# Performance work log

Measured on AMD Instinct MI355X. Metric: run time of the kernel, lower is better.

## Reference

```python
import jax, jax.numpy as jnp
import numpy as np
from jax import lax

B, CIN, IMG = 32, 3, 128   # batch, image channels, image size
D, K = 256, 512            # codebook dim, codebook size


def _conv(x, w, stride, pad):
    # PyTorch Conv2d (bias=False), NCHW / OIHW
    return lax.conv_general_dilated(x, w, (stride, stride), ((pad, pad), (pad, pad)),
                                    dimension_numbers=('NCHW', 'OIHW', 'NCHW'))


def _deconv(x, w, b):
    # PyTorch ConvTranspose2d(k=4, s=2, p=1): lhs_dilation=2, pad=k-1-p=2, flipped kernel,
    # weight layout (in, out, kh, kw) -> 'IOHW'
    y = lax.conv_general_dilated(x, jnp.flip(w, (2, 3)), (1, 1), ((2, 2), (2, 2)),
                                 lhs_dilation=(2, 2),
                                 dimension_numbers=('NCHW', 'IOHW', 'NCHW'))
    return y + b[None, :, None, None]


def _res(x, w1, w2):
    # Faithful to the source ResidualBlock: relu1 output is DISCARDED (conv1 applied to x)
    out = _conv(x, w1, 1, 1)      # 3x3, pad 1
    out = jax.nn.relu(out)
    out = _conv(out, w2, 1, 0)    # 1x1, pad 0
    return out + x


def setup_inputs() -> dict:
    key = jax.random.key(0)
    ks = jax.random.split(key, 20)
    s = 0.05
    inp = {
        'x': jax.random.uniform(ks[0], (B, CIN, IMG, IMG), jnp.float32),
        # codebook, init uniform(-1/K, 1/K) as in init_weights
        'embed_w': jax.random.uniform(ks[1], (K, D), jnp.float32, -1.0 / K, 1.0 / K),
        # encoder
        'e_w1': jax.random.normal(ks[2], (D, CIN, 4, 4), jnp.float32) * s,
        'e_w2': jax.random.normal(ks[3], (D, D, 4, 4), jnp.float32) * s,
        'e_r1a': jax.random.normal(ks[4], (D, D, 3, 3), jnp.float32) * s,
        'e_r1b': jax.random.normal(ks[5], (D, D, 1, 1), jnp.float32) * s,
        'e_r2a': jax.random.normal(ks[6], (D, D, 3, 3), jnp.float32) * s,
        'e_r2b': jax.random.normal(ks[7], (D, D, 1, 1), jnp.float32) * s,
        # decoder
        'd_r1a': jax.random.normal(ks[8], (D, D, 3, 3), jnp.float32) * s,
        'd_r1b': jax.random.normal(ks[9], (D, D, 1, 1), jnp.float32) * s,
        'd_r2a': jax.random.normal(ks[10], (D, D, 3, 3), jnp.float32) * s,
        'd_r2b': jax.random.normal(ks[11], (D, D, 1, 1), jnp.float32) * s,
        'dt1_w': jax.random.normal(ks[12], (D, D, 4, 4), jnp.float32) * s,  # (in,out,kh,kw)
        'dt1_b': jnp.zeros((D,), jnp.float32),
        'dt2_w': jax.random.normal(ks[13], (D, CIN, 4, 4), jnp.float32) * s,
        'dt2_b': jnp.zeros((CIN,), jnp.float32),
    }
    return inp


def reference(x, embed_w, e_w1, e_w2, e_r1a, e_r1b, e_r2a, e_r2b,
              d_r1a, d_r1b, d_r2a, d_r2b, dt1_w, dt1_b, dt2_w, dt2_b):
    # ---- encoder (BN layers exist but are never called in the source forward) ----
    h = jax.nn.relu(_conv(x, e_w1, 2, 1))          # (B,D,64,64)
    h = jax.nn.relu(_conv(h, e_w2, 2, 1))          # (B,D,32,32)
    h = _res(h, e_r1a, e_r1b)
    z_e = _res(h, e_r2a, e_r2b)                    # (B,D,H,W)

    # ---- vector quantisation ----
    ze = jnp.transpose(z_e, (0, 2, 3, 1))          # (B,H,W,D)
    # squared L2 distances via expansion (same argmin/values as the broadcast diff tensor)
    d2 = (jnp.sum(ze * ze, -1, keepdims=True)      # (B,H,W,1)
          - 2.0 * jnp.einsum('bhwd,kd->bhwk', ze, embed_w)
          + jnp.sum(embed_w * embed_w, -1))        # (B,H,W,K)
    dist = jnp.sqrt(jnp.maximum(d2, 0.0))          # torch.norm(p=2) before min
    idx = jnp.argmin(dist, axis=-1)                # (B,H,W)
    z_q = embed_w[idx]                             # (B,H,W,D) gather

    # losses: source averages over an extra duplicated K axis, identical to mean over B,H,W
    sg = lax.stop_gradient
    loss1 = jnp.mean(jnp.sum((ze - sg(z_q)) ** 2, -1))   # grads -> encoder
    loss2 = jnp.mean(jnp.sum((sg(ze) - z_q) ** 2, -1))   # grads -> codebook

    # ---- decoder (takes z_q; BN layers never called; relu after deconv1 only) ----
    dq = jnp.transpose(z_q, (0, 3, 1, 2))          # (B,D,H,W)
    dq = _res(dq, d_r1a, d_r1b)
    dq = _res(dq, d_r2a, d_r2b)
    dq = jax.nn.relu(_deconv(dq, dt1_w, dt1_b))    # (B,D,64,64)
    recon = jax.nn.sigmoid(_deconv(dq, dt2_w, dt2_b))  # (B,3,128,128)
    return recon, loss1, loss2
```

## Files before the change

### kernel.cpp

```cpp
#include <hip/hip_runtime.h>


typedef __attribute__((ext_vector_type(8))) short bf16x8;
typedef __attribute__((ext_vector_type(4))) float f32x4;
#define MFMA_B16(a, b, c) __builtin_amdgcn_mfma_f32_16x16x32_bf16(a, b, c, 0, 0, 0)

__device__ inline unsigned short f2b(float f) {
    unsigned int u = __float_as_uint(f);
    unsigned int r = u + 0x7fffu + ((u >> 16) & 1u);
    return (unsigned short)(r >> 16);
}
__device__ inline float b2f(unsigned short u) {
    return __uint_as_float(((unsigned int)u) << 16);
}

struct PermfArgs {
    const float* src[10];
    int kw[10];
    int so[10], si[10], sh[10], sw[10];
    int cum[11];
};

__global__ void permf_all_k(PermfArgs a, unsigned short* __restrict__ dst)
{
    int gid = blockIdx.x * 256 + threadIdx.x;
    if (gid >= a.cum[10]) return;
    int seg = 0;
    while (seg < 9 && gid >= a.cum[seg + 1]) ++seg;
    int l = gid - a.cum[seg];
    int q = l & 31;
    int n = (l >> 5) & 255;
    int rest = l >> 13;
    int cch = rest & 7;
    int khkw = rest >> 3;
    int kh = khkw / a.kw[seg], kw = khkw % a.kw[seg];
    int ci = cch * 32 + q;
    dst[gid] = f2b(a.src[seg][n * a.so[seg] + ci * a.si[seg] + kh * a.sh[seg] + kw * a.sw[seg]]);
}

__global__ void misc_prep_k(const float* __restrict__ dt2_w, unsigned short* __restrict__ wg,
                            const float* __restrict__ embed, unsigned short* __restrict__ embF,
                            const float* __restrict__ e_w1, unsigned short* __restrict__ wgc,
                            float* __restrict__ nrm)
{
    int blk = blockIdx.x, tid = threadIdx.x;
    if (blk < 48) {
        int idx = blk * 256 + tid;
        int q = idx & 31;
        int n = (idx >> 5) % 48;
        int cch = idx / (48 * 32);
        int ci = cch * 32 + q;
        int oc = n % 3, khkw = n / 3;
        int kh = khkw >> 2, kw = khkw & 3;
        wg[idx] = f2b(dt2_w[ci * 48 + oc * 16 + kh * 4 + kw]);
    } else if (blk < 560) {
        int idx = (blk - 48) * 256 + tid;
        int q = idx & 31;
        int n = (idx >> 5) & 511;
        int cch = idx >> 14;
        embF[idx] = f2b(embed[n * 256 + cch * 32 + q]);
    } else if (blk < 624) {
        int idx = (blk - 560) * 256 + tid;
        int q = idx & 31;
        int n = (idx >> 5) & 255;
        int kt = idx >> 13;
        int k = kt * 32 + q;
        float v = 0.f;
        if (k < 48) {
            int ci = k >> 4, kh = (k >> 2) & 3, kwv = k & 3;
            v = e_w1[n * 48 + ci * 16 + kh * 4 + kwv];
        }
        wgc[idx] = f2b(v);
    } else {
        int row = (blk - 624) * 4 + (tid >> 6);
        int lane = tid & 63;
        float s = 0.f;
        #pragma unroll
        for (int c = 0; c < 256; c += 64) {
            float v = embed[row * 256 + c + lane];
            s += v * v;
        }
        #pragma unroll
        for (int off = 1; off < 64; off <<= 1) s += __shfl_xor(s, off);
        if (lane == 0) nrm[row] = s;
    }
}

__global__ void lossfin_k(const float* __restrict__ lpart, float* __restrict__ out)
{
    __shared__ float red[256];
    int tid = threadIdx.x;
    float s = 0.f;
    #pragma unroll
    for (int i = 0; i < 16; ++i) s += lpart[tid * 16 + i];
    red[tid] = s;
    __syncthreads();
    for (int off = 128; off > 0; off >>= 1) {
        if (tid < off) red[tid] += red[tid + off];
        __syncthreads();
    }
    if (tid == 0) {
        float m = red[0] * (1.0f / 32768.0f);
        out[1572864] = m;
        out[1572865] = m;
    }
}

__global__ void __launch_bounds__(256, 4)
conv1m_k(const float* __restrict__ x, const unsigned short* __restrict__ wgc,
         unsigned short* __restrict__ out)
{
    int bh = blockIdx.x;
    int b = bh >> 6, oh = bh & 63;
    int tid = threadIdx.x;
    int lane = tid & 63, wv = tid >> 6;
    int m = lane & 15, quad = lane >> 4;
    __shared__ float xrow[3][4][130];
    __shared__ __align__(16) unsigned short imc[64 * 72];
    for (int s = tid; s < 1560; s += 256) {
        int col = s % 130;
        int t = s / 130;
        int r = t & 3;
        int c = t >> 2;
        int ih = 2 * oh - 1 + r, iw = col - 1;
        float v = 0.f;
        if ((unsigned)ih < 128u && (unsigned)iw < 128u)
            v = x[(((b * 3 + c) << 7) + ih) * 128 + iw];
        xrow[c][r][col] = v;
    }
    __syncthreads();
    for (int s = tid; s < 4096; s += 256) {
        int px = s >> 6, k = s & 63;
        float v = 0.f;
        if (k < 48) {
            int ci = k >> 4, kh = (k >> 2) & 3, kw = k & 3;
            v = xrow[ci][kh][2 * px + kw];
        }
        imc[px * 72 + k] = f2b(v);
    }
    __syncthreads();
    f32x4 acc[16];
    f32x4 z = {0.f, 0.f, 0.f, 0.f};
    #pragma unroll
    for (int i = 0; i < 16; ++i) acc[i] = z;
    bf16x8 a0 = *(const bf16x8*)&imc[((wv << 4) + m) * 72 + (quad << 3)];
    bf16x8 a1 = *(const bf16x8*)&imc[((wv << 4) + m) * 72 + 32 + (quad << 3)];
    #pragma unroll
    for (int nt = 0; nt < 16; ++nt) {
        bf16x8 b0 = *(const bf16x8*)&wgc[(nt * 16 + m) * 32 + (quad << 3)];
        bf16x8 b1 = *(const bf16x8*)&wgc[(256 + nt * 16 + m) * 32 + (quad << 3)];
        acc[nt] = MFMA_B16(a0, b0, acc[nt]);
        acc[nt] = MFMA_B16(a1, b1, acc[nt]);
    }
    #pragma unroll
    for (int nt = 0; nt < 16; ++nt)
        #pragma unroll
        for (int r = 0; r < 4; ++r) {
            int px = (wv << 4) + quad * 4 + r;
            out[(((bh << 6) + px) << 8) + nt * 16 + (lane & 15)] = f2b(fmaxf(acc[nt][r], 0.f));
        }
}

__global__ void __launch_bounds__(256, 3)
mconv2_k(const unsigned short* __restrict__ in, const unsigned short* __restrict__ wf,
         unsigned short* __restrict__ out)
{
    int blk = blockIdx.x;
    int bb = blk >> 4, j = blk & 15;
    int lane = threadIdx.x & 63;
    int n0 = (threadIdx.x >> 6) << 6;
    int m = lane & 15, quad = lane >> 4;
    __shared__ __align__(16) unsigned short win[2 * 66 * 132];
    f32x4 acc[2][2][4];
    f32x4 z = {0.f, 0.f, 0.f, 0.f};
    #pragma unroll
    for (int a = 0; a < 2; ++a)
        #pragma unroll
        for (int i = 0; i < 2; ++i)
            #pragma unroll
            for (int t = 0; t < 4; ++t) acc[a][i][t] = z;

    for (int c0 = 0; c0 < 256; c0 += 128) {
        for (int kh = 0; kh < 4; ++kh) {
            __syncthreads();
            for (int s = threadIdx.x; s < 2 * 66 * 16; s += 256) {
                int c16 = s & 15;
                int t2 = s >> 4;
                int col = t2 % 66;
                int rr = t2 / 66;
                int ih = 4 * j - 1 + kh + 2 * rr, iw = col - 1;
                int4 v = make_int4(0, 0, 0, 0);
                if ((unsigned)ih < 64u && (unsigned)iw < 64u)
                    v = *(const int4*)&in[((((bb << 6) + ih) << 6) + iw) * 256 + c0 + (c16 << 3)];
                int cs = (col >> 1) + (col & 1) * 33;
                *(int4*)&win[(rr * 66 + cs) * 132 + (c16 << 3)] = v;
            }
            __syncthreads();
            #pragma unroll
            for (int kw = 0; kw < 4; ++kw) {
                int csoff = (kw >> 1) + (kw & 1) * 33;
                #pragma unroll
                for (int cch = 0; cch < 4; ++cch) {
                    bf16x8 a00 = *(const bf16x8*)&win[(m + csoff) * 132 + (cch << 5) + (quad << 3)];
                    bf16x8 a01 = *(const bf16x8*)&win[(m + 16 + csoff) * 132 + (cch << 5) + (quad << 3)];
                    bf16x8 a10 = *(const bf16x8*)&win[(66 + m + csoff) * 132 + (cch << 5) + (quad << 3)];
                    bf16x8 a11 = *(const bf16x8*)&win[(66 + m + 16 + csoff) * 132 + (cch << 5) + (quad << 3)];
                    int cg = (c0 >> 5) + cch;
                    int wbase = ((((kh << 2) + kw) * 8 + cg) * 256 + n0 + m) * 32 + (quad << 3);
                    bf16x8 b0 = *(const bf16x8*)&wf[wbase];
                    bf16x8 b1 = *(const bf16x8*)&wf[wbase + 16 * 32];
                    bf16x8 b2 = *(const bf16x8*)&wf[wbase + 32 * 32];
                    bf16x8 b3 = *(const bf16x8*)&wf[wbase + 48 * 32];
                    acc[0][0][0] = MFMA_B16(a00, b0, acc[0][0][0]);
                    acc[0][0][1] = MFMA_B16(a00, b1, acc[0][0][1]);
                    acc[0][0][2] = MFMA_B16(a00, b2, acc[0][0][2]);
                    acc[0][0][3] = MFMA_B16(a00, b3, acc[0][0][3]);
                    acc[0][1][0] = MFMA_B16(a01, b0, acc[0][1][0]);
                    acc[0][1][1] = MFMA_B16(a01, b1, acc[0][1][1]);
                    acc[0][1][2] = MFMA_B16(a01, b2, acc[0][1][2]);
                    acc[0][1][3] = MFMA_B16(a01, b3, acc[0][1][3]);
                    acc[1][0][0] = MFMA_B16(a10, b0, acc[1][0][0]);
                    acc[1][0][1] = MFMA_B16(a10, b1, acc[1][0][1]);
                    acc[1][0][2] = MFMA_B16(a10, b2, acc[1][0][2]);
                    acc[1][0][3] = MFMA_B16(a10, b3, acc[1][0][3]);
                    acc[1][1][0] = MFMA_B16(a11, b0, acc[1][1][0]);
                    acc[1][1][1] = MFMA_B16(a11, b1, acc[1][1][1]);
                    acc[1][1][2] = MFMA_B16(a11, b2, acc[1][1][2]);
                    acc[1][1][3] = MFMA_B16(a11, b3, acc[1][1][3]);
                }
            }
        }
    }
    #pragma unroll
    for (int row = 0; row < 2; ++row) {
        int oh = 2 * j + row;
        #pragma unroll
        for (int mt = 0; mt < 2; ++mt)
            #pragma unroll
            for (int nt = 0; nt < 4; ++nt)
                #pragma unroll
                for (int r = 0; r < 4; ++r) {
                    int px = mt * 16 + quad * 4 + r;
                    int col = n0 + nt * 16 + m;
                    out[((((bb << 5) + oh) << 5) + px) * 256 + col] = f2b(fmaxf(acc[row][mt][nt][r], 0.f));
                }
    }
}

__global__ void __launch_bounds__(256, 4)
res3_k(const unsigned short* __restrict__ in, const unsigned short* __restrict__ wfA,
       const unsigned short* __restrict__ wfB, unsigned short* __restrict__ outb,
       float* __restrict__ outf, int f32out)
{
    int blk = blockIdx.x;
    int bb = blk >> 5, j = blk & 31;
    int tid = threadIdx.x;
    int lane = tid & 63;
    int n0 = (tid >> 6) << 6;
    int m = lane & 15, quad = lane >> 4;
    __shared__ __align__(16) unsigned short win[3 * 34 * 132];
    f32x4 acc[2][4];
    f32x4 z = {0.f, 0.f, 0.f, 0.f};
    #pragma unroll
    for (int i = 0; i < 2; ++i)
        #pragma unroll
        for (int t = 0; t < 4; ++t) acc[i][t] = z;

    for (int c0 = 0; c0 < 256; c0 += 128) {
        __syncthreads();
        for (int s = tid; s < 3 * 34 * 16; s += 256) {
            int c16 = s & 15;
            int t2 = s >> 4;
            int col = t2 % 34;
            int rr = t2 / 34;
            int ih = j - 1 + rr, iw = col - 1;
            int4 v = make_int4(0, 0, 0, 0);
            if ((unsigned)ih < 32u && (unsigned)iw < 32u)
                v = *(const int4*)&in[((((bb << 5) + ih) << 5) + iw) * 256 + c0 + (c16 << 3)];
            *(int4*)&win[(rr * 34 + col) * 132 + (c16 << 3)] = v;
        }
        __syncthreads();
        for (int kh = 0; kh < 3; ++kh) {
            #pragma unroll
            for (int kw = 0; kw < 3; ++kw) {
                #pragma unroll
                for (int cch = 0; cch < 4; ++cch) {
                    const unsigned short* ba = &win[(kh * 34 + m + kw) * 132 + (cch << 5) + (quad << 3)];
                    bf16x8 a0 = *(const bf16x8*)ba;
                    bf16x8 a1 = *(const bf16x8*)(ba + 16 * 132);
                    int cg = (c0 >> 5) + cch;
                    int wbase = (((kh * 3 + kw) * 8 + cg) * 256 + n0 + m) * 32 + (quad << 3);
                    bf16x8 b0 = *(const bf16x8*)&wfA[wbase];
                    bf16x8 b1 = *(const bf16x8*)&wfA[wbase + 16 * 32];
                    bf16x8 b2 = *(const bf16x8*)&wfA[wbase + 32 * 32];
                    bf16x8 b3 = *(const bf16x8*)&wfA[wbase + 48 * 32];
                    acc[0][0] = MFMA_B16(a0, b0, acc[0][0]);
                    acc[0][1] = MFMA_B16(a0, b1, acc[0][1]);
                    acc[0][2] = MFMA_B16(a0, b2, acc[0][2]);
                    acc[0][3] = MFMA_B16(a0, b3, acc[0][3]);
                    acc[1][0] = MFMA_B16(a1, b0, acc[1][0]);
                    acc[1][1] = MFMA_B16(a1, b1, acc[1][1]);
                    acc[1][2] = MFMA_B16(a1, b2, acc[1][2]);
                    acc[1][3] = MFMA_B16(a1, b3, acc[1][3]);
                }
            }
        }
    }

    __syncthreads();
    #pragma unroll
    for (int i = 0; i < 2; ++i)
        #pragma unroll
        for (int nt = 0; nt < 4; ++nt)
            #pragma unroll
            for (int r = 0; r < 4; ++r) {
                int p = i * 16 + quad * 4 + r;
                win[p * 264 + n0 + nt * 16 + m] = f2b(fmaxf(acc[i][nt][r], 0.f));
            }
    __syncthreads();

    f32x4 acc2[2][4];
    #pragma unroll
    for (int i = 0; i < 2; ++i)
        #pragma unroll
        for (int t = 0; t < 4; ++t) acc2[i][t] = z;

    #pragma unroll
    for (int cch = 0; cch < 8; ++cch) {
        bf16x8 a0 = *(const bf16x8*)&win[m * 264 + (cch << 5) + (quad << 3)];
        bf16x8 a1 = *(const bf16x8*)&win[(m + 16) * 264 + (cch << 5) + (quad << 3)];
        int wbase = (cch * 256 + n0 + m) * 32 + (quad << 3);
        bf16x8 b0 = *(const bf16x8*)&wfB[wbase];
        bf16x8 b1 = *(const bf16x8*)&wfB[wbase + 16 * 32];
        bf16x8 b2 = *(const bf16x8*)&wfB[wbase + 32 * 32];
        bf16x8 b3 = *(const bf16x8*)&wfB[wbase + 48 * 32];
        acc2[0][0] = MFMA_B16(a0, b0, acc2[0][0]);
        acc2[0][1] = MFMA_B16(a0, b1, acc2[0][1]);
        acc2[0][2] = MFMA_B16(a0, b2, acc2[0][2]);
        acc2[0][3] = MFMA_B16(a0, b3, acc2[0][3]);
        acc2[1][0] = MFMA_B16(a1, b0, acc2[1][0]);
        acc2[1][1] = MFMA_B16(a1, b1, acc2[1][1]);
        acc2[1][2] = MFMA_B16(a1, b2, acc2[1][2]);
        acc2[1][3] = MFMA_B16(a1, b3, acc2[1][3]);
    }

    float* winf = (float*)win;
    int rowbase = blk << 13;
    #pragma unroll
    for (int half = 0; half < 2; ++half) {
        __syncthreads();
        #pragma unroll
        for (int nt = 0; nt < 4; ++nt)
            #pragma unroll
            for (int r = 0; r < 4; ++r) {
                int pxl = quad * 4 + r;
                winf[pxl * 260 + n0 + nt * 16 + m] = acc2[half][nt][r];
            }
        __syncthreads();
        #pragma unroll
        for (int k = 0; k < 2; ++k) {
            int s = tid + k * 256;
            int pxl = s >> 5;
            int c8 = s & 31;
            int px = half * 16 + pxl;
            int idx = rowbase + (px << 8) + (c8 << 3);
            int4 rv = *(const int4*)&in[idx];
            const float* wp = &winf[pxl * 260 + (c8 << 3)];
            float v0 = wp[0] + b2f((unsigned short)((unsigned)rv.x & 0xffffu));
            float v1 = wp[1] + b2f((unsigned short)((unsigned)rv.x >> 16));
            float v2 = wp[2] + b2f((unsigned short)((unsigned)rv.y & 0xffffu));
            float v3 = wp[3] + b2f((unsigned short)((unsigned)rv.y >> 16));
            float v4 = wp[4] + b2f((unsigned short)((unsigned)rv.z & 0xffffu));
            float v5 = wp[5] + b2f((unsigned short)((unsigned)rv.z >> 16));
            float v6 = wp[6] + b2f((unsigned short)((unsigned)rv.w & 0xffffu));
            float v7 = wp[7] + b2f((unsigned short)((unsigned)rv.w >> 16));
            unsigned w0 = (unsigned)f2b(v0) | ((unsigned)f2b(v1) << 16);
            unsigned w1 = (unsigned)f2b(v2) | ((unsigned)f2b(v3) << 16);
            unsigned w2 = (unsigned)f2b(v4) | ((unsigned)f2b(v5) << 16);
            unsigned w3 = (unsigned)f2b(v6) | ((unsigned)f2b(v7) << 16);
            *(int4*)&outb[idx] = make_int4((int)w0, (int)w1, (int)w2, (int)w3);
            if (f32out) {
                *(float4*)&outf[idx]     = make_float4(v0, v1, v2, v3);
                *(float4*)&outf[idx + 4] = make_float4(v4, v5, v6, v7);
            }
        }
    }
}

__global__ void __launch_bounds__(256, 3)
mdeconv1_k(const unsigned short* __restrict__ in, const unsigned short* __restrict__ wf,
           const float* __restrict__ bias, unsigned short* __restrict__ out)
{
    int blk = blockIdx.x;
    int bb = blk >> 5;
    int rem = blk & 31;
    int pp = rem >> 4;
    int i = rem & 15;
    int oy_a = pp + 4 * i;
    int p = (oy_a + 1) & 1;
    int r0a = (oy_a + 1 - p) >> 1;
    int rbase = r0a - 1;
    int tid = threadIdx.x;
    int lane = tid & 63;
    int n0 = (tid >> 6) << 6;
    int m = lane & 15, quad = lane >> 4;
    __shared__ __align__(16) unsigned short win[3 * 34 * 264];
    __shared__ __align__(16) unsigned short tb[16 * 264];

    for (int s = tid; s < 3 * 34 * 32; s += 256) {
        int c8 = s & 31;
        int t2 = s >> 5;
        int col = t2 % 34;
        int rr = t2 / 34;
        int ih = rbase + rr, iw = col - 1;
        int4 v = make_int4(0, 0, 0, 0);
        if ((unsigned)ih < 32u && (unsigned)iw < 32u)
            v = *(const int4*)&in[((((bb << 5) + ih) << 5) + iw) * 256 + (c8 << 3)];
        *(int4*)&win[(rr * 34 + col) * 264 + (c8 << 3)] = v;
    }
    __syncthreads();

    for (int par = 0; par < 2; ++par) {
        f32x4 acc[2][2][4];
        f32x4 z = {0.f, 0.f, 0.f, 0.f};
        #pragma unroll
        for (int a = 0; a < 2; ++a)
            #pragma unroll
            for (int i2 = 0; i2 < 2; ++i2)
                #pragma unroll
                for (int t = 0; t < 4; ++t) acc[a][i2][t] = z;

        #pragma unroll
        for (int t = 0; t < 2; ++t) {
            int kh = p + 2 * t;
            #pragma unroll
            for (int u = 0; u < 2; ++u) {
                int kw = (1 - par) + 2 * u;
                int ixoff = par - u + 1;
                #pragma unroll
                for (int cch = 0; cch < 8; ++cch) {
                    const unsigned short* baA = &win[((1 - t) * 34 + m + ixoff) * 264 + (cch << 5) + (quad << 3)];
                    const unsigned short* baB = baA + 34 * 264;
                    bf16x8 a00 = *(const bf16x8*)baA;
                    bf16x8 a01 = *(const bf16x8*)(baA + 16 * 264);
                    bf16x8 a10 = *(const bf16x8*)baB;
                    bf16x8 a11 = *(const bf16x8*)(baB + 16 * 264);
                    int wbase = ((((kh << 2) + kw) * 8 + cch) * 256 + n0 + m) * 32 + (quad << 3);
                    bf16x8 b0 = *(const bf16x8*)&wf[wbase];
                    bf16x8 b1 = *(const bf16x8*)&wf[wbase + 16 * 32];
                    bf16x8 b2 = *(const bf16x8*)&wf[wbase + 32 * 32];
                    bf16x8 b3 = *(const bf16x8*)&wf[wbase + 48 * 32];
                    acc[0][0][0] = MFMA_B16(a00, b0, acc[0][0][0]);
                    acc[0][0][1] = MFMA_B16(a00, b1, acc[0][0][1]);
                    acc[0][0][2] = MFMA_B16(a00, b2, acc[0][0][2]);
                    acc[0][0][3] = MFMA_B16(a00, b3, acc[0][0][3]);
                    acc[0][1][0] = MFMA_B16(a01, b0, acc[0][1][0]);
                    acc[0][1][1] = MFMA_B16(a01, b1, acc[0][1][1]);
                    acc[0][1][2] = MFMA_B16(a01, b2, acc[0][1][2]);
                    acc[0][1][3] = MFMA_B16(a01, b3, acc[0][1][3]);
                    acc[1][0][0] = MFMA_B16(a10, b0, acc[1][0][0]);
                    acc[1][0][1] = MFMA_B16(a10, b1, acc[1][0][1]);
                    acc[1][0][2] = MFMA_B16(a10, b2, acc[1][0][2]);
                    acc[1][0][3] = MFMA_B16(a10, b3, acc[1][0][3]);
                    acc[1][1][0] = MFMA_B16(a11, b0, acc[1][1][0]);
                    acc[1][1][1] = MFMA_B16(a11, b1, acc[1][1][1]);
                    acc[1][1][2] = MFMA_B16(a11, b2, acc[1][1][2]);
                    acc[1][1][3] = MFMA_B16(a11, b3, acc[1][1][3]);
                }
            }
        }

        #pragma unroll
        for (int row = 0; row < 2; ++row) {
            int oy = oy_a + 2 * row;
            #pragma unroll
            for (int mt = 0; mt < 2; ++mt) {
                __syncthreads();
                #pragma unroll
                for (int nt = 0; nt < 4; ++nt) {
                    float bs = bias[n0 + nt * 16 + m];
                    #pragma unroll
                    for (int rr = 0; rr < 4; ++rr) {
                        float v = fmaxf(acc[row][mt][nt][rr] + bs, 0.f);
                        tb[(quad * 4 + rr) * 264 + n0 + nt * 16 + m] = f2b(v);
                    }
                }
                __syncthreads();
                #pragma unroll
                for (int k = 0; k < 2; ++k) {
                    int s = tid + k * 256;
                    int pxl = s >> 5;
                    int c8 = s & 31;
                    int ox = 2 * (mt * 16 + pxl) + par;
                    *(int4*)&out[((((bb << 6) + oy) << 6) + ox) * 256 + (c8 << 3)] =
                        *(const int4*)&tb[pxl * 264 + (c8 << 3)];
                }
            }
        }
    }
}

__global__ void __launch_bounds__(256, 2)
vqm_k(const unsigned short* __restrict__ zeb, const float* __restrict__ zef,
      const unsigned short* __restrict__ embF, const float* __restrict__ embed,
      const float* __restrict__ nrm, unsigned short* __restrict__ zq,
      float* __restrict__ lpart)
{
    int bh = blockIdx.x;
    int tid = threadIdx.x;
    int lane = tid & 63;
    int wv = tid >> 6;
    int m = lane & 15, quad = lane >> 4;
    __shared__ __align__(16) unsigned short win[32 * 264];
    __shared__ float bvv[4][32];
    __shared__ int   bii[4][32];
    __shared__ int   bidx[32];
    int rowbase = bh << 13;
    for (int s = tid; s < 32 * 32; s += 256) {
        int c8 = s & 31, px = s >> 5;
        *(int4*)&win[px * 264 + (c8 << 3)] = *(const int4*)&zeb[rowbase + (px << 8) + (c8 << 3)];
    }
    __syncthreads();

    f32x4 acc[2][8];
    f32x4 z = {0.f, 0.f, 0.f, 0.f};
    #pragma unroll
    for (int i = 0; i < 2; ++i)
        #pragma unroll
        for (int j = 0; j < 8; ++j) acc[i][j] = z;

    #pragma unroll
    for (int cch = 0; cch < 8; ++cch) {
        bf16x8 a0 = *(const bf16x8*)&win[m * 264 + (cch << 5) + (quad << 3)];
        bf16x8 a1 = *(const bf16x8*)&win[(m + 16) * 264 + (cch << 5) + (quad << 3)];
        #pragma unroll
        for (int nt = 0; nt < 8; ++nt) {
            bf16x8 b = *(const bf16x8*)&embF[((cch << 9) + (wv << 7) + (nt << 4) + m) * 32 + (quad << 3)];
            acc[0][nt] = MFMA_B16(a0, b, acc[0][nt]);
            acc[1][nt] = MFMA_B16(a1, b, acc[1][nt]);
        }
    }

    float nv[8];
    #pragma unroll
    for (int nt = 0; nt < 8; ++nt) nv[nt] = nrm[(wv << 7) + (nt << 4) + m];

    #pragma unroll
    for (int mt = 0; mt < 2; ++mt)
        #pragma unroll
        for (int r = 0; r < 4; ++r) {
            float bv = 1e30f;
            int bi = 0x7fffffff;
            #pragma unroll
            for (int nt = 0; nt < 8; ++nt) {
                float d = nv[nt] - 2.f * acc[mt][nt][r];
                int n = (wv << 7) + (nt << 4) + m;
                if (d < bv || (d == bv && n < bi)) { bv = d; bi = n; }
            }
            #pragma unroll
            for (int off = 1; off < 16; off <<= 1) {
                float ov = __shfl_xor(bv, off);
                int oi = __shfl_xor(bi, off);
                if (ov < bv || (ov == bv && oi < bi)) { bv = ov; bi = oi; }
            }
            if (m == 0) {
                int px = mt * 16 + quad * 4 + r;
                bvv[wv][px] = bv;
                bii[wv][px] = bi;
            }
        }
    __syncthreads();
    if (tid < 32) {
        float bv = bvv[0][tid];
        int bi = bii[0][tid];
        #pragma unroll
        for (int w2 = 1; w2 < 4; ++w2) {
            float ov = bvv[w2][tid];
            int oi = bii[w2][tid];
            if (ov < bv || (ov == bv && oi < bi)) { bv = ov; bi = oi; }
        }
        bidx[tid] = bi;
    }
    __syncthreads();

    float lsum = 0.f;
    #pragma unroll
    for (int j = 0; j < 8; ++j) {
        int px = (wv << 3) + j;
        int bi = bidx[px];
        int pix = (bh << 5) + px;
        const float4 e = *(const float4*)&embed[bi * 256 + (lane << 2)];
        const float4 zv = *(const float4*)&zef[(pix << 8) + (lane << 2)];
        ushort4 eq;
        eq.x = f2b(e.x); eq.y = f2b(e.y); eq.z = f2b(e.z); eq.w = f2b(e.w);
        *(ushort4*)&zq[(pix << 8) + (lane << 2)] = eq;
        float dx = zv.x - e.x, dy = zv.y - e.y, dz = zv.z - e.z, dw = zv.w - e.w;
        lsum += dx * dx + dy * dy + dz * dz + dw * dw;
    }
    #pragma unroll
    for (int off = 1; off < 64; off <<= 1) lsum += __shfl_xor(lsum, off);
    if (lane == 0) lpart[(bh << 2) + wv] = lsum;
}

__global__ void __launch_bounds__(256, 4)
mdec2a_k(const unsigned short* __restrict__ in, const unsigned short* __restrict__ wg,
         float* __restrict__ Y)
{
    int tid = threadIdx.x;
    int lane = tid & 63;
    int wv = tid >> 6;
    int m = lane & 15, quad = lane >> 4;
    __shared__ __align__(16) unsigned short win[64 * 264];
    int pxbase = blockIdx.x << 6;
    for (int s = tid; s < 64 * 32; s += 256) {
        int c8 = s & 31, px = s >> 5;
        *(int4*)&win[px * 264 + (c8 << 3)] = *(const int4*)&in[((pxbase + px) << 8) + (c8 << 3)];
    }
    __syncthreads();
    f32x4 acc[3];
    f32x4 z = {0.f, 0.f, 0.f, 0.f};
    acc[0] = z; acc[1] = z; acc[2] = z;
    #pragma unroll
    for (int cch = 0; cch < 8; ++cch) {
        bf16x8 a = *(const bf16x8*)&win[((wv << 4) + m) * 264 + (cch << 5) + (quad << 3)];
        #pragma unroll
        for (int nt = 0; nt < 3; ++nt) {
            bf16x8 b = *(const bf16x8*)&wg[(cch * 48 + nt * 16 + m) * 32 + (quad << 3)];
            acc[nt] = MFMA_B16(a, b, acc[nt]);
        }
    }
    #pragma unroll
    for (int nt = 0; nt < 3; ++nt)
        #pragma unroll
        for (int r = 0; r < 4; ++r) {
            int px = pxbase + (wv << 4) + quad * 4 + r;
            Y[px * 48 + nt * 16 + m] = acc[nt][r];
        }
}

__global__ void dec2b_k(const float* __restrict__ Y, const float* __restrict__ bias,
                        float* __restrict__ out)
{
    int idx = blockIdx.x * 256 + threadIdx.x;
    int b = idx >> 14;
    int rem = idx & 16383;
    int oy = rem >> 7;
    int ox = rem & 127;
    int p = (oy + 1) & 1;
    int q = (ox + 1) & 1;
    float acc0 = bias[0], acc1 = bias[1], acc2 = bias[2];
    #pragma unroll
    for (int t = 0; t < 2; ++t) {
        int kh = p + 2 * t;
        int ih = (oy + 1 - kh) >> 1;
        if ((unsigned)ih >= 64u) continue;
        #pragma unroll
        for (int u = 0; u < 2; ++u) {
            int kw = q + 2 * u;
            int iw = (ox + 1 - kw) >> 1;
            if ((unsigned)iw >= 64u) continue;
            int base = ((((b << 6) + ih) << 6) + iw) * 48 + ((kh << 2) + kw) * 3;
            acc0 += Y[base];
            acc1 += Y[base + 1];
            acc2 += Y[base + 2];
        }
    }
    int obase = (b * 3 << 14) + (oy << 7) + ox;
    out[obase]           = 1.f / (1.f + expf(-acc0));
    out[obase + 16384]   = 1.f / (1.f + expf(-acc1));
    out[obase + 32768]   = 1.f / (1.f + expf(-acc2));
}

extern "C" void kernel_launch(void* const* d_in, const int* in_sizes, int n_in,
                              void* d_out, int out_size, void* d_ws, size_t ws_size,
                              hipStream_t stream)
{
    (void)in_sizes; (void)n_in; (void)out_size; (void)ws_size;
    const float* x      = (const float*)d_in[0];
    const float* embed  = (const float*)d_in[1];
    const float* e_w1   = (const float*)d_in[2];
    const float* e_w2   = (const float*)d_in[3];
    const float* e_r1a  = (const float*)d_in[4];
    const float* e_r1b  = (const float*)d_in[5];
    const float* e_r2a  = (const float*)d_in[6];
    const float* e_r2b  = (const float*)d_in[7];
    const float* d_r1a  = (const float*)d_in[8];
    const float* d_r1b  = (const float*)d_in[9];
    const float* d_r2a  = (const float*)d_in[10];
    const float* d_r2b  = (const float*)d_in[11];
    const float* dt1_w  = (const float*)d_in[12];
    const float* dt1_b  = (const float*)d_in[13];
    const float* dt2_w  = (const float*)d_in[14];
    const float* dt2_b  = (const float*)d_in[15];
    float* outp = (float*)d_out;

    char* base = (char*)d_ws;
    size_t off = 0;
    auto alloc = [&](size_t bytes) { char* p = base + off; off += (bytes + 255) & ~size_t(255); return p; };
    unsigned short* A0b = (unsigned short*)alloc(67108864);
    float*          A1f = (float*)alloc(33554432);
    unsigned short* L0  = (unsigned short*)alloc(16777216);
    unsigned short* L1  = (unsigned short*)alloc(16777216);
    unsigned short* L2  = (unsigned short*)alloc(16777216);
    unsigned short* Wf  = (unsigned short*)alloc(9437184);
    unsigned short* Wg  = (unsigned short*)alloc(24576);
    unsigned short* EmbF = (unsigned short*)alloc(262144);
    unsigned short* WgC = (unsigned short*)alloc(32768);
    float* Nrm  = (float*)alloc(2048);
    float* Lpart = (float*)alloc(16384);
    float* Y = A1f;
    (void)L2;

    unsigned short* Wf_ew2  = Wf;
    unsigned short* Wf_er1a = Wf + 1048576;
    unsigned short* Wf_er1b = Wf + 1638400;
    unsigned short* Wf_er2a = Wf + 1703936;
    unsigned short* Wf_er2b = Wf + 2293760;
    unsigned short* Wf_dr1a = Wf + 2359296;
    unsigned short* Wf_dr1b = Wf + 2949120;
    unsigned short* Wf_dr2a = Wf + 3014656;
    unsigned short* Wf_dr2b = Wf + 3604480;
    unsigned short* Wf_dt1  = Wf + 3670016;

    PermfArgs pa;
    const float* srcs[10] = {e_w2, e_r1a, e_r1b, e_r2a, e_r2b, d_r1a, d_r1b, d_r2a, d_r2b, dt1_w};
    int kws[10] = {4, 3, 1, 3, 1, 3, 1, 3, 1, 4};
    int sos[10] = {4096, 2304, 256, 2304, 256, 2304, 256, 2304, 256, 16};
    int sis[10] = {16, 9, 1, 9, 1, 9, 1, 9, 1, 4096};
    int shs[10] = {4, 3, 0, 3, 0, 3, 0, 3, 0, 4};
    int sws[10] = {1, 1, 0, 1, 0, 1, 0, 1, 0, 1};
    int cums[11] = {0, 1048576, 1638400, 1703936, 2293760, 2359296,
                    2949120, 3014656, 3604480, 3670016, 4718592};
    for (int k = 0; k < 10; ++k) {
        pa.src[k] = srcs[k]; pa.kw[k] = kws[k]; pa.so[k] = sos[k];
        pa.si[k] = sis[k]; pa.sh[k] = shs[k]; pa.sw[k] = sws[k];
        pa.cum[k] = cums[k];
    }
    pa.cum[10] = cums[10];

    permf_all_k<<<18432, 256, 0, stream>>>(pa, Wf);
    misc_prep_k<<<752, 256, 0, stream>>>(dt2_w, Wg, embed, EmbF, e_w1, WgC, Nrm);

    conv1m_k<<<32 * 64, 256, 0, stream>>>(x, WgC, A0b);
    mconv2_k<<<32 * 16, 256, 0, stream>>>(A0b, Wf_ew2, L1);
    res3_k<<<32 * 32, 256, 0, stream>>>(L1, Wf_er1a, Wf_er1b, L0, nullptr, 0);
    res3_k<<<32 * 32, 256, 0, stream>>>(L0, Wf_er2a, Wf_er2b, L1, A1f, 1);

    vqm_k<<<32 * 32, 256, 0, stream>>>(L1, A1f, EmbF, embed, Nrm, L1, Lpart);

    res3_k<<<32 * 32, 256, 0, stream>>>(L1, Wf_dr1a, Wf_dr1b, L0, nullptr, 0);
    res3_k<<<32 * 32, 256, 0, stream>>>(L0, Wf_dr2a, Wf_dr2b, L1, nullptr, 0);
    mdeconv1_k<<<32 * 32, 256, 0, stream>>>(L1, Wf_dt1, dt1_b, A0b);
    mdec2a_k<<<2048, 256, 0, stream>>>(A0b, Wg, Y);
    dec2b_k<<<2048, 256, 0, stream>>>(Y, dt2_b, outp);
    lossfin_k<<<1, 256, 0, stream>>>(Lpart, outp);
}
```

Before: 713.7 us.

## Stage all 256 channels per kh in LDS and prefetch weights in mconv2

The encoder's second conv kernel now loads the full 256-channel input window for each kernel row into shared memory at once, instead of two 128-channel halves. This halves the number of barrier/staging rounds. The inner loop is flattened to 32 iterations and software-prefetches the next iteration's weight fragments from global memory into registers while the current MFMAs run. In exchange, shared memory doubles to about 70 KB and register pressure rises, so launch bounds drop from 3 to 2 blocks per SM, which lowers occupancy.

```diff
diff --git a/kernel.cpp b/kernel.cpp
--- a/kernel.cpp
+++ b/kernel.cpp
@@ -161,7 +161,7 @@
         }
 }
 
-__global__ void __launch_bounds__(256, 3)
+__global__ void __launch_bounds__(256, 2)
 mconv2_k(const unsigned short* __restrict__ in, const unsigned short* __restrict__ wf,
          unsigned short* __restrict__ out)
 {
@@ -170,7 +170,7 @@
     int lane = threadIdx.x & 63;
     int n0 = (threadIdx.x >> 6) << 6;
     int m = lane & 15, quad = lane >> 4;
-    __shared__ __align__(16) unsigned short win[2 * 66 * 132];
+    __shared__ __align__(16) unsigned short win[2 * 66 * 264];
     f32x4 acc[2][2][4];
     f32x4 z = {0.f, 0.f, 0.f, 0.f};
     #pragma unroll
@@ -180,55 +180,63 @@
             #pragma unroll
             for (int t = 0; t < 4; ++t) acc[a][i][t] = z;
 
-    for (int c0 = 0; c0 < 256; c0 += 128) {
-        for (int kh = 0; kh < 4; ++kh) {
-            __syncthreads();
-            for (int s = threadIdx.x; s < 2 * 66 * 16; s += 256) {
-                int c16 = s & 15;
-                int t2 = s >> 4;
-                int col = t2 % 66;
-                int rr = t2 / 66;
-                int ih = 4 * j - 1 + kh + 2 * rr, iw = col - 1;
-                int4 v = make_int4(0, 0, 0, 0);
-                if ((unsigned)ih < 64u && (unsigned)iw < 64u)
-                    v = *(const int4*)&in[((((bb << 6) + ih) << 6) + iw) * 256 + c0 + (c16 << 3)];
-                int cs = (col >> 1) + (col & 1) * 33;
-                *(int4*)&win[(rr * 66 + cs) * 132 + (c16 << 3)] = v;
-            }
-            __syncthreads();
-            #pragma unroll
-            for (int kw = 0; kw < 4; ++kw) {
-                int csoff = (kw >> 1) + (kw & 1) * 33;
-                #pragma unroll
-                for (int cch = 0; cch < 4; ++cch) {
-                    bf16x8 a00 = *(const bf16x8*)&win[(m + csoff) * 132 + (cch << 5) + (quad << 3)];
-                    bf16x8 a01 = *(const bf16x8*)&win[(m + 16 + csoff) * 132 + (cch << 5) + (quad << 3)];
-                    bf16x8 a10 = *(const bf16x8*)&win[(66 + m + csoff) * 132 + (cch << 5) + (quad << 3)];
-                    bf16x8 a11 = *(const bf16x8*)&win[(66 + m + 16 + csoff) * 132 + (cch << 5) + (quad << 3)];
-                    int cg = (c0 >> 5) + cch;
-                    int wbase = ((((kh << 2) + kw) * 8 + cg) * 256 + n0 + m) * 32 + (quad << 3);
-                    bf16x8 b0 = *(const bf16x8*)&wf[wbase];
-                    bf16x8 b1 = *(const bf16x8*)&wf[wbase + 16 * 32];
-                    bf16x8 b2 = *(const bf16x8*)&wf[wbase + 32 * 32];
-                    bf16x8 b3 = *(const bf16x8*)&wf[wbase + 48 * 32];
-                    acc[0][0][0] = MFMA_B16(a00, b0, acc[0][0][0]);
-                    acc[0][0][1] = MFMA_B16(a00, b1, acc[0][0][1]);
-                    acc[0][0][2] = MFMA_B16(a00, b2, acc[0][0][2]);
-                    acc[0][0][3] = MFMA_B16(a00, b3, acc[0][0][3]);
-                    acc[0][1][0] = MFMA_B16(a01, b0, acc[0][1][0]);
-                    acc[0][1][1] = MFMA_B16(a01, b1, acc[0][1][1]);
-                    acc[0][1][2] = MFMA_B16(a01, b2, acc[0][1][2]);
-                    acc[0][1][3] = MFMA_B16(a01, b3, acc[0][1][3]);
-                    acc[1][0][0] = MFMA_B16(a10, b0, acc[1][0][0]);
-                    acc[1][0][1] = MFMA_B16(a10, b1, acc[1][0][1]);
-                    acc[1][0][2] = MFMA_B16(a10, b2, acc[1][0][2]);
-                    acc[1][0][3] = MFMA_B16(a10, b3, acc[1][0][3]);
-                    acc[1][1][0] = MFMA_B16(a11, b0, acc[1][1][0]);
-                    acc[1][1][1] = MFMA_B16(a11, b1, acc[1][1][1]);
-                    acc[1][1][2] = MFMA_B16(a11, b2, acc[1][1][2]);
-                    acc[1][1][3] = MFMA_B16(a11, b3, acc[1][1][3]);
-                }
-            }
+    for (int kh = 0; kh < 4; ++kh) {
+        __syncthreads();
+        for (int s = threadIdx.x; s < 2 * 66 * 32; s += 256) {
+            int c32 = s & 31;
+            int t2 = s >> 5;
+            int col = t2 % 66;
+            int rr = t2 / 66;
+            int ih = 4 * j - 1 + kh + 2 * rr, iw = col - 1;
+            int4 v = make_int4(0, 0, 0, 0);
+            if ((unsigned)ih < 64u && (unsigned)iw < 64u)
+                v = *(const int4*)&in[((((bb << 6) + ih) << 6) + iw) * 256 + (c32 << 3)];
+            int cs = (col >> 1) + (col & 1) * 33;
+            *(int4*)&win[(rr * 66 + cs) * 264 + (c32 << 3)] = v;
+        }
+        __syncthreads();
+        int wb0 = (((kh << 2) + 0) * 8 + 0) * 256;
+        const unsigned short* wrow = &wf[(wb0 + n0 + m) * 32 + (quad << 3)];
+        bf16x8 nb0 = *(const bf16x8*)wrow;
+        bf16x8 nb1 = *(const bf16x8*)(wrow + 16 * 32);
+        bf16x8 nb2 = *(const bf16x8*)(wrow + 32 * 32);
+        bf16x8 nb3 = *(const bf16x8*)(wrow + 48 * 32);
+        #pragma unroll
+        for (int it = 0; it < 32; ++it) {
+            bf16x8 cb0 = nb0, cb1 = nb1, cb2 = nb2, cb3 = nb3;
+            if (it < 31) {
+                int it2 = it + 1;
+                int kw2 = it2 >> 3, cch2 = it2 & 7;
+                const unsigned short* wp =
+                    &wf[((((kh << 2) + kw2) * 8 + cch2) * 256 + n0 + m) * 32 + (quad << 3)];
+                nb0 = *(const bf16x8*)wp;
+                nb1 = *(const bf16x8*)(wp + 16 * 32);
+                nb2 = *(const bf16x8*)(wp + 32 * 32);
+                nb3 = *(const bf16x8*)(wp + 48 * 32);
+            }
+            int kw = it >> 3, cch = it & 7;
+            int csoff = (kw >> 1) + (kw & 1) * 33;
+            const unsigned short* ba = &win[(m + csoff) * 264 + (cch << 5) + (quad << 3)];
+            bf16x8 a00 = *(const bf16x8*)ba;
+            bf16x8 a01 = *(const bf16x8*)(ba + 16 * 264);
+            bf16x8 a10 = *(const bf16x8*)(ba + 66 * 264);
+            bf16x8 a11 = *(const bf16x8*)(ba + 82 * 264);
+            acc[0][0][0] = MFMA_B16(a00, cb0, acc[0][0][0]);
+            acc[0][0][1] = MFMA_B16(a00, cb1, acc[0][0][1]);
+            acc[0][0][2] = MFMA_B16(a00, cb2, acc[0][0][2]);
+            acc[0][0][3] = MFMA_B16(a00, cb3, acc[0][0][3]);
+            acc[0][1][0] = MFMA_B16(a01, cb0, acc[0][1][0]);
+            acc[0][1][1] = MFMA_B16(a01, cb1, acc[0][1][1]);
+            acc[0][1][2] = MFMA_B16(a01, cb2, acc[0][1][2]);
+            acc[0][1][3] = MFMA_B16(a01, cb3, acc[0][1][3]);
+            acc[1][0][0] = MFMA_B16(a10, cb0, acc[1][0][0]);
+            acc[1][0][1] = MFMA_B16(a10, cb1, acc[1][0][1]);
+            acc[1][0][2] = MFMA_B16(a10, cb2, acc[1][0][2]);
+            acc[1][0][3] = MFMA_B16(a10, cb3, acc[1][0][3]);
+            acc[1][1][0] = MFMA_B16(a11, cb0, acc[1][1][0]);
+            acc[1][1][1] = MFMA_B16(a11, cb1, acc[1][1][1]);
+            acc[1][1][2] = MFMA_B16(a11, cb2, acc[1][1][2]);
+            acc[1][1][3] = MFMA_B16(a11, cb3, acc[1][1][3]);
         }
     }
     #pragma unroll
```

New measurement: 710.0 us. Within noise of the previous version (-0.5%).

## Prefetch next input window into registers during MFMA compute in conv kernels

Applied to the files above, without the earlier changes.

In mconv2_k and res3_k, the next slab of input rows or channels is now loaded from global memory into registers while the MFMA loop runs on the current LDS window. After a barrier the registers are written to LDS. mconv2_k also widens its LDS window to all 256 channels per kh step, which halves the number of load/sync phases, and lowers its launch bound from 3 to 2 blocks per unit. This hides global load latency behind compute, at the cost of higher register pressure (17 int4 prefetch registers), larger LDS use and possibly lower occupancy.

```diff
diff --git a/kernel.cpp b/kernel.cpp
--- a/kernel.cpp
+++ b/kernel.cpp
@@ -161,16 +161,17 @@
         }
 }
 
-__global__ void __launch_bounds__(256, 3)
+__global__ void __launch_bounds__(256, 2)
 mconv2_k(const unsigned short* __restrict__ in, const unsigned short* __restrict__ wf,
          unsigned short* __restrict__ out)
 {
     int blk = blockIdx.x;
     int bb = blk >> 4, j = blk & 15;
-    int lane = threadIdx.x & 63;
-    int n0 = (threadIdx.x >> 6) << 6;
+    int tid = threadIdx.x;
+    int lane = tid & 63;
+    int n0 = (tid >> 6) << 6;
     int m = lane & 15, quad = lane >> 4;
-    __shared__ __align__(16) unsigned short win[2 * 66 * 132];
+    __shared__ __align__(16) unsigned short win[2 * 66 * 264];
     f32x4 acc[2][2][4];
     f32x4 z = {0.f, 0.f, 0.f, 0.f};
     #pragma unroll
@@ -180,55 +181,100 @@
             #pragma unroll
             for (int t = 0; t < 4; ++t) acc[a][i][t] = z;
 
-    for (int c0 = 0; c0 < 256; c0 += 128) {
-        for (int kh = 0; kh < 4; ++kh) {
+    int4 rv[17];
+
+    #pragma unroll
+    for (int k = 0; k < 17; ++k) {
+        int s = tid + (k << 8);
+        rv[k] = make_int4(0, 0, 0, 0);
+        if (s < 4224) {
+            int c32 = s & 31;
+            int t2 = s >> 5;
+            int col = t2 % 66;
+            int rr = t2 / 66;
+            int ih = 4 * j - 1 + 2 * rr, iw = col - 1;
+            if ((unsigned)ih < 64u && (unsigned)iw < 64u)
+                rv[k] = *(const int4*)&in[((((bb << 6) + ih) << 6) + iw) * 256 + (c32 << 3)];
+        }
+    }
+    #pragma unroll
+    for (int k = 0; k < 17; ++k) {
+        int s = tid + (k << 8);
+        if (s < 4224) {
+            int c32 = s & 31;
+            int t2 = s >> 5;
+            int col = t2 % 66;
+            int rr = t2 / 66;
+            int cs = (col >> 1) + (col & 1) * 33;
+            *(int4*)&win[(rr * 66 + cs) * 264 + (c32 << 3)] = rv[k];
+        }
+    }
+    __syncthreads();
+
+    for (int kh = 0; kh < 4; ++kh) {
+        if (kh < 3) {
+            #pragma unroll
+            for (int k = 0; k < 17; ++k) {
+                int s = tid + (k << 8);
+                rv[k] = make_int4(0, 0, 0, 0);
+                if (s < 4224) {
+                    int c32 = s & 31;
+                    int t2 = s >> 5;
+                    int col = t2 % 66;
+                    int rr = t2 / 66;
+                    int ih = 4 * j + kh + 2 * rr, iw = col - 1;
+                    if ((unsigned)ih < 64u && (unsigned)iw < 64u)
+                        rv[k] = *(const int4*)&in[((((bb << 6) + ih) << 6) + iw) * 256 + (c32 << 3)];
+                }
+            }
+        }
+        for (int kw = 0; kw < 4; ++kw) {
+            int csoff = (kw >> 1) + (kw & 1) * 33;
+            #pragma unroll
+            for (int cch = 0; cch < 8; ++cch) {
+                const unsigned short* ba = &win[(m + csoff) * 264 + (cch << 5) + (quad << 3)];
+                bf16x8 a00 = *(const bf16x8*)ba;
+                bf16x8 a01 = *(const bf16x8*)(ba + 16 * 264);
+                bf16x8 a10 = *(const bf16x8*)(ba + 66 * 264);
+                bf16x8 a11 = *(const bf16x8*)(ba + 82 * 264);
+                int wbase = ((((kh << 2) + kw) * 8 + cch) * 256 + n0 + m) * 32 + (quad << 3);
+                bf16x8 b0 = *(const bf16x8*)&wf[wbase];
+                bf16x8 b1 = *(const bf16x8*)&wf[wbase + 16 * 32];
+                bf16x8 b2 = *(const bf16x8*)&wf[wbase + 32 * 32];
+                bf16x8 b3 = *(const bf16x8*)&wf[wbase + 48 * 32];
+                acc[0][0][0] = MFMA_B16(a00, b0, acc[0][0][0]);
+                acc[0][0][1] = MFMA_B16(a00, b1, acc[0][0][1]);
+                acc[0][0][2] = MFMA_B16(a00, b2, acc[0][0][2]);
+                acc[0][0][3] = MFMA_B16(a00, b3, acc[0][0][3]);
+                acc[0][1][0] = MFMA_B16(a01, b0, acc[0][1][0]);
+                acc[0][1][1] = MFMA_B16(a01, b1, acc[0][1][1]);
+                acc[0][1][2] = MFMA_B16(a01, b2, acc[0][1][2]);
+                acc[0][1][3] = MFMA_B16(a01, b3, acc[0][1][3]);
+                acc[1][0][0] = MFMA_B16(a10, b0, acc[1][0][0]);
+                acc[1][0][1] = MFMA_B16(a10, b1, acc[1][0][1]);
+                acc[1][0][2] = MFMA_B16(a10, b2, acc[1][0][2]);
+                acc[1][0][3] = MFMA_B16(a10, b3, acc[1][0][3]);
+                acc[1][1][0] = MFMA_B16(a11, b0, acc[1][1][0]);
+                acc[1][1][1] = MFMA_B16(a11, b1, acc[1][1][1]);
+                acc[1][1][2] = MFMA_B16(a11, b2, acc[1][1][2]);
+                acc[1][1][3] = MFMA_B16(a11, b3, acc[1][1][3]);
+            }
+        }
+        __syncthreads();
+        if (kh < 3) {
+            #pragma unroll
+            for (int k = 0; k < 17; ++k) {
+                int s = tid + (k << 8);
+                if (s < 4224) {
+                    int c32 = s & 31;
+                    int t2 = s >> 5;
+                    int col = t2 % 66;
+                    int rr = t2 / 66;
+                    int cs = (col >> 1) + (col & 1) * 33;
+                    *(int4*)&win[(rr * 66 + cs) * 264 + (c32 << 3)] = rv[k];
+                }
+            }
             __syncthreads();
-            for (int s = threadIdx.x; s < 2 * 66 * 16; s += 256) {
-                int c16 = s & 15;
-                int t2 = s >> 4;
-                int col = t2 % 66;
-                int rr = t2 / 66;
-                int ih = 4 * j - 1 + kh + 2 * rr, iw = col - 1;
-                int4 v = make_int4(0, 0, 0, 0);
-                if ((unsigned)ih < 64u && (unsigned)iw < 64u)
-                    v = *(const int4*)&in[((((bb << 6) + ih) << 6) + iw) * 256 + c0 + (c16 << 3)];
-                int cs = (col >> 1) + (col & 1) * 33;
-                *(int4*)&win[(rr * 66 + cs) * 132 + (c16 << 3)] = v;
-            }
-            __syncthreads();
-            #pragma unroll
-            for (int kw = 0; kw < 4; ++kw) {
-                int csoff = (kw >> 1) + (kw & 1) * 33;
-                #pragma unroll
-                for (int cch = 0; cch < 4; ++cch) {
-                    bf16x8 a00 = *(const bf16x8*)&win[(m + csoff) * 132 + (cch << 5) + (quad << 3)];
-                    bf16x8 a01 = *(const bf16x8*)&win[(m + 16 + csoff) * 132 + (cch << 5) + (quad << 3)];
-                    bf16x8 a10 = *(const bf16x8*)&win[(66 + m + csoff) * 132 + (cch << 5) + (quad << 3)];
-                    bf16x8 a11 = *(const bf16x8*)&win[(66 + m + 16 + csoff) * 132 + (cch << 5) + (quad << 3)];
-                    int cg = (c0 >> 5) + cch;
-                    int wbase = ((((kh << 2) + kw) * 8 + cg) * 256 + n0 + m) * 32 + (quad << 3);
-                    bf16x8 b0 = *(const bf16x8*)&wf[wbase];
-                    bf16x8 b1 = *(const bf16x8*)&wf[wbase + 16 * 32];
-                    bf16x8 b2 = *(const bf16x8*)&wf[wbase + 32 * 32];
-                    bf16x8 b3 = *(const bf16x8*)&wf[wbase + 48 * 32];
-                    acc[0][0][0] = MFMA_B16(a00, b0, acc[0][0][0]);
-                    acc[0][0][1] = MFMA_B16(a00, b1, acc[0][0][1]);
-                    acc[0][0][2] = MFMA_B16(a00, b2, acc[0][0][2]);
-                    acc[0][0][3] = MFMA_B16(a00, b3, acc[0][0][3]);
-                    acc[0][1][0] = MFMA_B16(a01, b0, acc[0][1][0]);
-                    acc[0][1][1] = MFMA_B16(a01, b1, acc[0][1][1]);
-                    acc[0][1][2] = MFMA_B16(a01, b2, acc[0][1][2]);
-                    acc[0][1][3] = MFMA_B16(a01, b3, acc[0][1][3]);
-                    acc[1][0][0] = MFMA_B16(a10, b0, acc[1][0][0]);
-                    acc[1][0][1] = MFMA_B16(a10, b1, acc[1][0][1]);
-                    acc[1][0][2] = MFMA_B16(a10, b2, acc[1][0][2]);
-                    acc[1][0][3] = MFMA_B16(a10, b3, acc[1][0][3]);
-                    acc[1][1][0] = MFMA_B16(a11, b0, acc[1][1][0]);
-                    acc[1][1][1] = MFMA_B16(a11, b1, acc[1][1][1]);
-                    acc[1][1][2] = MFMA_B16(a11, b2, acc[1][1][2]);
-                    acc[1][1][3] = MFMA_B16(a11, b3, acc[1][1][3]);
-                }
-            }
         }
     }
     #pragma unroll
@@ -266,20 +312,52 @@
         #pragma unroll
         for (int t = 0; t < 4; ++t) acc[i][t] = z;
 
-    for (int c0 = 0; c0 < 256; c0 += 128) {
-        __syncthreads();
-        for (int s = tid; s < 3 * 34 * 16; s += 256) {
+    int4 rv[7];
+
+    #pragma unroll
+    for (int k = 0; k < 7; ++k) {
+        int s = tid + (k << 8);
+        rv[k] = make_int4(0, 0, 0, 0);
+        if (s < 1632) {
             int c16 = s & 15;
             int t2 = s >> 4;
             int col = t2 % 34;
             int rr = t2 / 34;
             int ih = j - 1 + rr, iw = col - 1;
-            int4 v = make_int4(0, 0, 0, 0);
             if ((unsigned)ih < 32u && (unsigned)iw < 32u)
-                v = *(const int4*)&in[((((bb << 5) + ih) << 5) + iw) * 256 + c0 + (c16 << 3)];
-            *(int4*)&win[(rr * 34 + col) * 132 + (c16 << 3)] = v;
-        }
-        __syncthreads();
+                rv[k] = *(const int4*)&in[((((bb << 5) + ih) << 5) + iw) * 256 + (c16 << 3)];
+        }
+    }
+    #pragma unroll
+    for (int k = 0; k < 7; ++k) {
+        int s = tid + (k << 8);
+        if (s < 1632) {
+            int c16 = s & 15;
+            int t2 = s >> 4;
+            int col = t2 % 34;
+            int rr = t2 / 34;
+            *(int4*)&win[(rr * 34 + col) * 132 + (c16 << 3)] = rv[k];
+        }
+    }
+    __syncthreads();
+
+    for (int ph = 0; ph < 2; ++ph) {
+        if (ph == 0) {
+            #pragma unroll
+            for (int k = 0; k < 7; ++k) {
+                int s = tid + (k << 8);
+                rv[k] = make_int4(0, 0, 0, 0);
+                if (s < 1632) {
+                    int c16 = s & 15;
+                    int t2 = s >> 4;
+                    int col = t2 % 34;
+                    int rr = t2 / 34;
+                    int ih = j - 1 + rr, iw = col - 1;
+                    if ((unsigned)ih < 32u && (unsigned)iw < 32u)
+                        rv[k] = *(const int4*)&in[((((bb << 5) + ih) << 5) + iw) * 256 + 128 + (c16 << 3)];
+                }
+            }
+        }
         for (int kh = 0; kh < 3; ++kh) {
             #pragma unroll
             for (int kw = 0; kw < 3; ++kw) {
@@ -288,7 +366,7 @@
                     const unsigned short* ba = &win[(kh * 34 + m + kw) * 132 + (cch << 5) + (quad << 3)];
                     bf16x8 a0 = *(const bf16x8*)ba;
                     bf16x8 a1 = *(const bf16x8*)(ba + 16 * 132);
-                    int cg = (c0 >> 5) + cch;
+                    int cg = ph * 4 + cch;
                     int wbase = (((kh * 3 + kw) * 8 + cg) * 256 + n0 + m) * 32 + (quad << 3);
                     bf16x8 b0 = *(const bf16x8*)&wfA[wbase];
                     bf16x8 b1 = *(const bf16x8*)&wfA[wbase + 16 * 32];
@@ -305,9 +383,23 @@
                 }
             }
         }
-    }
-
-    __syncthreads();
+        __syncthreads();
+        if (ph == 0) {
+            #pragma unroll
+            for (int k = 0; k < 7; ++k) {
+                int s = tid + (k << 8);
+                if (s < 1632) {
+                    int c16 = s & 15;
+                    int t2 = s >> 4;
+                    int col = t2 % 34;
+                    int rr = t2 / 34;
+                    *(int4*)&win[(rr * 34 + col) * 132 + (c16 << 3)] = rv[k];
+                }
+            }
+            __syncthreads();
+        }
+    }
+
     #pragma unroll
     for (int i = 0; i < 2; ++i)
         #pragma unroll
@@ -364,16 +456,16 @@
             int c8 = s & 31;
             int px = half * 16 + pxl;
             int idx = rowbase + (px << 8) + (c8 << 3);
-            int4 rv = *(const int4*)&in[idx];
+            int4 rvv = *(const int4*)&in[idx];
             const float* wp = &winf[pxl * 260 + (c8 << 3)];
-            float v0 = wp[0] + b2f((unsigned short)((unsigned)rv.x & 0xffffu));
-            float v1 = wp[1] + b2f((unsigned short)((unsigned)rv.x >> 16));
-            float v2 = wp[2] + b2f((unsigned short)((unsigned)rv.y & 0xffffu));
-            float v3 = wp[3] + b2f((unsigned short)((unsigned)rv.y >> 16));
-            float v4 = wp[4] + b2f((unsigned short)((unsigned)rv.z & 0xffffu));
-            float v5 = wp[5] + b2f((unsigned short)((unsigned)rv.z >> 16));
-            float v6 = wp[6] + b2f((unsigned short)((unsigned)rv.w & 0xffffu));
-            float v7 = wp[7] + b2f((unsigned short)((unsigned)rv.w >> 16));
+            float v0 = wp[0] + b2f((unsigned short)((unsigned)rvv.x & 0xffffu));
+            float v1 = wp[1] + b2f((unsigned short)((unsigned)rvv.x >> 16));
+            float v2 = wp[2] + b2f((unsigned short)((unsigned)rvv.y & 0xffffu));
+            float v3 = wp[3] + b2f((unsigned short)((unsigned)rvv.y >> 16));
+            float v4 = wp[4] + b2f((unsigned short)((unsigned)rvv.z & 0xffffu));
+            float v5 = wp[5] + b2f((unsigned short)((unsigned)rvv.z >> 16));
+            float v6 = wp[6] + b2f((unsigned short)((unsigned)rvv.w & 0xffffu));
+            float v7 = wp[7] + b2f((unsigned short)((unsigned)rvv.w >> 16));
             unsigned w0 = (unsigned)f2b(v0) | ((unsigned)f2b(v1) << 16);
             unsigned w1 = (unsigned)f2b(v2) | ((unsigned)f2b(v3) << 16);
             unsigned w2 = (unsigned)f2b(v4) | ((unsigned)f2b(v5) << 16);
```

New measurement: 703.5 us. No clear change (-1.4%).
